# Kernel tuning notes

Hardware: AMD Instinct MI355X
Metric: run time of the kernel (lower is better)

The kernel has to match this reference:

```python
import jax, jax.numpy as jnp
import numpy as np

NEG = -1e6  # mask fill value used by d2l-style masked_softmax


def setup_inputs() -> dict:
    key = jax.random.key(0)
    kq, kk, kv, kl = jax.random.split(key, 4)
    B, Lq, Lk, D = 8, 2048, 2048, 64
    Q = jax.random.normal(kq, (B, Lq, D), dtype=jnp.float32)
    K = jax.random.normal(kk, (B, Lk, D), dtype=jnp.float32)
    V = jax.random.normal(kv, (B, Lk, D), dtype=jnp.float32)
    valid_len = jax.random.randint(kl, (B,), 1, Lk + 1, dtype=jnp.int64)
    return {"Q": Q, "K": K, "V": V, "valid_len": valid_len}


def reference(Q, K, V, valid_len):
    d = Q.shape[-1]
    scale = 1.0 / jnp.sqrt(jnp.asarray(d, dtype=Q.dtype))
    # scores: [B, Lq, Lk]
    S = jnp.einsum('bqd,bkd->bqk', Q, K) * scale
    Lk = K.shape[1]
    # per-batch key-length mask: position j valid iff j < valid_len[b]
    mask = jnp.arange(Lk)[None, None, :] < valid_len[:, None, None]
    S = jnp.where(mask, S, NEG)
    A = jax.nn.softmax(S, axis=-1)
    return jnp.einsum('bqk,bkd->bqd', A, V)
```

## Files before the change

### kernel.cpp

```cpp
#include <hip/hip_runtime.h>
#include <hip/hip_bf16.h>


constexpr int B_  = 8;
constexpr int L_  = 2048;
constexpr int D_  = 64;
constexpr int BQ  = 128;
constexpr int BK  = 64;
constexpr int LDK = 72;
constexpr int NQ  = L_ / BQ;

constexpr float QSCALE = 0.125f * 1.44269504088896340736f;

using bf16x8 = __attribute__((ext_vector_type(8))) __bf16;
using f32x4  = __attribute__((ext_vector_type(4))) float;

union frag_u { unsigned u[4]; bf16x8 v; };

#if __has_builtin(__builtin_amdgcn_exp2f)
#define EXP2(x) __builtin_amdgcn_exp2f(x)
#else
#define EXP2(x) exp2f(x)
#endif

__device__ __forceinline__ unsigned pack2(float lo, float hi) {
    __hip_bfloat162 h = __float22bfloat162_rn(make_float2(lo, hi));
    return *(unsigned*)&h;
}
__device__ __forceinline__ int sniff_valid(const int* vl, int b) {
    const int p1 = vl[1];
    return (p1 == 0) ? vl[2 * b] : vl[b];
}

__global__ __launch_bounds__(256, 2) void attn_fwd(
    const float* __restrict__ Q, const float* __restrict__ K,
    const float* __restrict__ V, const int* __restrict__ vl,
    float* __restrict__ O, float* __restrict__ Opart,
    float* __restrict__ lpart, int nsplit, int splitk)
{
    __shared__ __align__(16) unsigned short Ks[BK * LDK];
    __shared__ __align__(16) unsigned short Vt[D_ * LDK];
    __shared__ __align__(16) unsigned short Ps[4 * 32 * LDK];

    const int id   = blockIdx.x;
    const int qt   = id & (NQ - 1);
    const int b    = (id >> 4) & (B_ - 1);
    const int s    = id >> 7;
    const int tid  = threadIdx.x;
    const int wave = tid >> 6;
    const int lan  = tid & 15;
    const int quad = (tid >> 4) & 3;

    const int valid  = sniff_valid(vl, b);
    const int kstart = s * splitk;
    if (kstart >= valid) return;
    const int kend   = min(kstart + splitk, valid);
    const int ntiles = (kend - kstart + BK - 1) / BK;

    const float* Kg = K + (size_t)b * L_ * D_;
    const float* Vg = V + (size_t)b * L_ * D_;

    const int krow = tid >> 4, kc0 = (tid & 15) * 4;
    const int vk0  = (tid & 31) * 2, vd0 = (tid >> 5) * 8;

    float4 kr[4], vr[4];
    {
        const float* ks = Kg + (size_t)(kstart + krow) * D_ + kc0;
        #pragma unroll
        for (int p = 0; p < 4; ++p) kr[p] = *(const float4*)(ks + (size_t)p * 16 * D_);
        const float* vs = Vg + (size_t)(kstart + vk0) * D_ + vd0;
        vr[0] = *(const float4*)(vs);
        vr[1] = *(const float4*)(vs + 4);
        vr[2] = *(const float4*)(vs + D_);
        vr[3] = *(const float4*)(vs + D_ + 4);
    }

    bf16x8 aq[2][2];
    #pragma unroll
    for (int g = 0; g < 2; ++g) {
        const float* qs = Q + ((size_t)b * L_ + qt * BQ + wave * 32 + g * 16 + lan) * D_;
        float4 q0 = *(const float4*)(qs + quad * 8);
        float4 q1 = *(const float4*)(qs + quad * 8 + 4);
        float4 q2 = *(const float4*)(qs + 32 + quad * 8);
        float4 q3 = *(const float4*)(qs + 32 + quad * 8 + 4);
        frag_u f0, f1;
        f0.u[0] = pack2(q0.x * QSCALE, q0.y * QSCALE);
        f0.u[1] = pack2(q0.z * QSCALE, q0.w * QSCALE);
        f0.u[2] = pack2(q1.x * QSCALE, q1.y * QSCALE);
        f0.u[3] = pack2(q1.z * QSCALE, q1.w * QSCALE);
        f1.u[0] = pack2(q2.x * QSCALE, q2.y * QSCALE);
        f1.u[1] = pack2(q2.z * QSCALE, q2.w * QSCALE);
        f1.u[2] = pack2(q3.x * QSCALE, q3.y * QSCALE);
        f1.u[3] = pack2(q3.z * QSCALE, q3.w * QSCALE);
        aq[g][0] = f0.v;
        aq[g][1] = f1.v;
    }

    f32x4 oacc[2][4];
    #pragma unroll
    for (int g = 0; g < 2; ++g)
        #pragma unroll
        for (int c = 0; c < 4; ++c) oacc[g][c] = (f32x4){0.f, 0.f, 0.f, 0.f};
    float lsum[2] = {0.f, 0.f};

    unsigned short* Pw = &Ps[wave * 32 * LDK];

    for (int t = 0; t < ntiles; ++t) {
        const int kt = kstart + t * BK;
        __syncthreads();

        #pragma unroll
        for (int p = 0; p < 4; ++p) {
            uint2 w = make_uint2(pack2(kr[p].x, kr[p].y), pack2(kr[p].z, kr[p].w));
            *(uint2*)&Ks[(p * 16 + krow) * LDK + kc0] = w;
        }
        {
            const float* a = (const float*)&vr[0];
            const float* c = (const float*)&vr[2];
            #pragma unroll
            for (int j = 0; j < 8; ++j)
                *(unsigned*)&Vt[(vd0 + j) * LDK + vk0] = pack2(a[j], c[j]);
        }
        __syncthreads();

        if (t + 1 < ntiles) {
            const int kn = kt + BK;
            const float* ks = Kg + (size_t)(kn + krow) * D_ + kc0;
            #pragma unroll
            for (int p = 0; p < 4; ++p) kr[p] = *(const float4*)(ks + (size_t)p * 16 * D_);
            const float* vs = Vg + (size_t)(kn + vk0) * D_ + vd0;
            vr[0] = *(const float4*)(vs);
            vr[1] = *(const float4*)(vs + 4);
            vr[2] = *(const float4*)(vs + D_);
            vr[3] = *(const float4*)(vs + D_ + 4);
        }

        #pragma unroll
        for (int c = 0; c < 4; ++c) {
            bf16x8 ak0 = *(const bf16x8*)&Ks[(c*16 + lan) * LDK + quad * 8];
            bf16x8 ak1 = *(const bf16x8*)&Ks[(c*16 + lan) * LDK + 32 + quad * 8];
            f32x4 z0 = (f32x4){0.f, 0.f, 0.f, 0.f};
            f32x4 z1 = (f32x4){0.f, 0.f, 0.f, 0.f};
            z0 = __builtin_amdgcn_mfma_f32_16x16x32_bf16(ak0, aq[0][0], z0, 0, 0, 0);
            z1 = __builtin_amdgcn_mfma_f32_16x16x32_bf16(ak0, aq[1][0], z1, 0, 0, 0);
            z0 = __builtin_amdgcn_mfma_f32_16x16x32_bf16(ak1, aq[0][1], z0, 0, 0, 0);
            z1 = __builtin_amdgcn_mfma_f32_16x16x32_bf16(ak1, aq[1][1], z1, 0, 0, 0);

            const int kbase = kt + c * 16 + quad * 4;
            float p0[4], p1[4];
            #pragma unroll
            for (int r = 0; r < 4; ++r) {
                const bool ok = (kbase + r) < valid;
                p0[r] = ok ? EXP2(z0[r]) : 0.f;
                p1[r] = ok ? EXP2(z1[r]) : 0.f;
                lsum[0] += p0[r];
                lsum[1] += p1[r];
            }
            *(uint2*)&Pw[lan * LDK + c * 16 + quad * 4] =
                make_uint2(pack2(p0[0], p0[1]), pack2(p0[2], p0[3]));
            *(uint2*)&Pw[(16 + lan) * LDK + c * 16 + quad * 4] =
                make_uint2(pack2(p1[0], p1[1]), pack2(p1[2], p1[3]));
        }

        bf16x8 ap[2][2];
        #pragma unroll
        for (int g = 0; g < 2; ++g) {
            ap[g][0] = *(const bf16x8*)&Pw[(g*16 + lan) * LDK + quad * 8];
            ap[g][1] = *(const bf16x8*)&Pw[(g*16 + lan) * LDK + 32 + quad * 8];
        }
        #pragma unroll
        for (int c = 0; c < 4; ++c) {
            bf16x8 bv0 = *(const bf16x8*)&Vt[(c*16 + lan) * LDK + quad * 8];
            bf16x8 bv1 = *(const bf16x8*)&Vt[(c*16 + lan) * LDK + 32 + quad * 8];
            #pragma unroll
            for (int g = 0; g < 2; ++g) {
                oacc[g][c] = __builtin_amdgcn_mfma_f32_16x16x32_bf16(ap[g][0], bv0, oacc[g][c], 0, 0, 0);
                oacc[g][c] = __builtin_amdgcn_mfma_f32_16x16x32_bf16(ap[g][1], bv1, oacc[g][c], 0, 0, 0);
            }
        }
    }

    #pragma unroll
    for (int g = 0; g < 2; ++g) {
        lsum[g] += __shfl_xor(lsum[g], 16);
        lsum[g] += __shfl_xor(lsum[g], 32);
    }

    const int rowbase = qt * BQ + wave * 32;
    if (nsplit == 1) {
        #pragma unroll
        for (int g = 0; g < 2; ++g) {
            float inv[4];
            #pragma unroll
            for (int r = 0; r < 4; ++r)
                inv[r] = 1.0f / __shfl(lsum[g], quad * 4 + r);
            float* Og = O + ((size_t)b * L_ + rowbase + g * 16) * D_;
            #pragma unroll
            for (int c = 0; c < 4; ++c)
                #pragma unroll
                for (int r = 0; r < 4; ++r)
                    Og[(size_t)(quad * 4 + r) * D_ + c * 16 + lan] = oacc[g][c][r] * inv[r];
        }
    } else {
        #pragma unroll
        for (int g = 0; g < 2; ++g) {
            float* Og = Opart + ((size_t)s * B_ * L_ + (size_t)b * L_ + rowbase + g * 16) * D_;
            #pragma unroll
            for (int c = 0; c < 4; ++c)
                #pragma unroll
                for (int r = 0; r < 4; ++r)
                    Og[(size_t)(quad * 4 + r) * D_ + c * 16 + lan] = oacc[g][c][r];
            if (quad == 0)
                lpart[(size_t)s * B_ * L_ + (size_t)b * L_ + rowbase + g * 16 + lan] = lsum[g];
        }
    }
}

__global__ __launch_bounds__(256) void attn_combine(
    const float* __restrict__ Opart, const float* __restrict__ lpart,
    const int* __restrict__ vl, float* __restrict__ O,
    int nsplit, int splitk)
{
    const int idx = blockIdx.x * 256 + threadIdx.x;
    const int row = idx >> 4;
    const int b   = row >> 11;
    const int off = (idx & 15) * 4;
    const int valid = sniff_valid(vl, b);
    const int ns = min(nsplit, (valid + splitk - 1) / splitk);

    float Lsum = 0.f;
    float4 acc = make_float4(0.f, 0.f, 0.f, 0.f);
    for (int s = 0; s < ns; ++s) {
        Lsum += lpart[s * (B_ * L_) + row];
        float4 o4 = *(const float4*)&Opart[(size_t)s * (B_ * L_ * D_) + (size_t)row * D_ + off];
        acc.x += o4.x; acc.y += o4.y; acc.z += o4.z; acc.w += o4.w;
    }
    const float inv = 1.0f / Lsum;
    acc.x *= inv; acc.y *= inv; acc.z *= inv; acc.w *= inv;
    *(float4*)&O[(size_t)row * D_ + off] = acc;
}

extern "C" void kernel_launch(void* const* d_in, const int* in_sizes, int n_in,
                              void* d_out, int out_size, void* d_ws, size_t ws_size,
                              hipStream_t stream) {
    const float* Q  = (const float*)d_in[0];
    const float* K  = (const float*)d_in[1];
    const float* V  = (const float*)d_in[2];
    const int*   vl = (const int*)d_in[3];
    float* O = (float*)d_out;

    auto need = [](int n) {
        return (size_t)n * (B_ * L_ * D_ + B_ * L_) * sizeof(float);
    };
    int nsplit = 1;
    if      (ws_size >= need(4)) nsplit = 4;
    else if (ws_size >= need(2)) nsplit = 2;
    const int splitk = L_ / nsplit;

    float* Opart = (float*)d_ws;
    float* lpart = Opart + (size_t)nsplit * B_ * L_ * D_;

    attn_fwd<<<dim3(nsplit * B_ * NQ), 256, 0, stream>>>(
        Q, K, V, vl, O, Opart, lpart, nsplit, splitk);
    if (nsplit > 1)
        attn_combine<<<dim3((B_ * L_ * D_ / 4) / 256), 256, 0, stream>>>(
            Opart, lpart, vl, O, nsplit, splitk);
}
```

Baseline: 88.38 us.

## Use a persistent atomic work queue and allow an eight-way key split

The attention kernel becomes persistent. A fixed grid of 512 blocks pulls (split, batch, q-tile) work items from a global atomic ticket, which is zeroed with a memset before each launch. Items whose key range starts past the batch's valid length are skipped cheaply, so the blocks balance the uneven per-batch work dynamically. The key split can now go to 8 when the workspace allows. That gives finer-grained items, but more partial-output traffic and a longer combine pass, plus an extra memset and atomic per item.

```diff
diff --git a/kernel.cpp b/kernel.cpp
--- a/kernel.cpp
+++ b/kernel.cpp
@@ -9,6 +9,7 @@
 constexpr int BK  = 64;
 constexpr int LDK = 72;
 constexpr int NQ  = L_ / BQ;
+constexpr int NBLK = 512;
 
 constexpr float QSCALE = 0.125f * 1.44269504088896340736f;
 
@@ -36,183 +37,201 @@
     const float* __restrict__ Q, const float* __restrict__ K,
     const float* __restrict__ V, const int* __restrict__ vl,
     float* __restrict__ O, float* __restrict__ Opart,
-    float* __restrict__ lpart, int nsplit, int splitk)
+    float* __restrict__ lpart, int* __restrict__ ticket,
+    int nsplit, int splitk)
 {
     __shared__ __align__(16) unsigned short Ks[BK * LDK];
     __shared__ __align__(16) unsigned short Vt[D_ * LDK];
     __shared__ __align__(16) unsigned short Ps[4 * 32 * LDK];
-
-    const int id   = blockIdx.x;
-    const int qt   = id & (NQ - 1);
-    const int b    = (id >> 4) & (B_ - 1);
-    const int s    = id >> 7;
+    __shared__ int sh_item;
+
     const int tid  = threadIdx.x;
     const int wave = tid >> 6;
     const int lan  = tid & 15;
     const int quad = (tid >> 4) & 3;
 
-    const int valid  = sniff_valid(vl, b);
-    const int kstart = s * splitk;
-    if (kstart >= valid) return;
-    const int kend   = min(kstart + splitk, valid);
-    const int ntiles = (kend - kstart + BK - 1) / BK;
-
-    const float* Kg = K + (size_t)b * L_ * D_;
-    const float* Vg = V + (size_t)b * L_ * D_;
-
     const int krow = tid >> 4, kc0 = (tid & 15) * 4;
     const int vk0  = (tid & 31) * 2, vd0 = (tid >> 5) * 8;
 
-    float4 kr[4], vr[4];
-    {
-        const float* ks = Kg + (size_t)(kstart + krow) * D_ + kc0;
-        #pragma unroll
-        for (int p = 0; p < 4; ++p) kr[p] = *(const float4*)(ks + (size_t)p * 16 * D_);
-        const float* vs = Vg + (size_t)(kstart + vk0) * D_ + vd0;
-        vr[0] = *(const float4*)(vs);
-        vr[1] = *(const float4*)(vs + 4);
-        vr[2] = *(const float4*)(vs + D_);
-        vr[3] = *(const float4*)(vs + D_ + 4);
-    }
-
-    bf16x8 aq[2][2];
-    #pragma unroll
-    for (int g = 0; g < 2; ++g) {
-        const float* qs = Q + ((size_t)b * L_ + qt * BQ + wave * 32 + g * 16 + lan) * D_;
-        float4 q0 = *(const float4*)(qs + quad * 8);
-        float4 q1 = *(const float4*)(qs + quad * 8 + 4);
-        float4 q2 = *(const float4*)(qs + 32 + quad * 8);
-        float4 q3 = *(const float4*)(qs + 32 + quad * 8 + 4);
-        frag_u f0, f1;
-        f0.u[0] = pack2(q0.x * QSCALE, q0.y * QSCALE);
-        f0.u[1] = pack2(q0.z * QSCALE, q0.w * QSCALE);
-        f0.u[2] = pack2(q1.x * QSCALE, q1.y * QSCALE);
-        f0.u[3] = pack2(q1.z * QSCALE, q1.w * QSCALE);
-        f1.u[0] = pack2(q2.x * QSCALE, q2.y * QSCALE);
-        f1.u[1] = pack2(q2.z * QSCALE, q2.w * QSCALE);
-        f1.u[2] = pack2(q3.x * QSCALE, q3.y * QSCALE);
-        f1.u[3] = pack2(q3.z * QSCALE, q3.w * QSCALE);
-        aq[g][0] = f0.v;
-        aq[g][1] = f1.v;
-    }
-
-    f32x4 oacc[2][4];
-    #pragma unroll
-    for (int g = 0; g < 2; ++g)
-        #pragma unroll
-        for (int c = 0; c < 4; ++c) oacc[g][c] = (f32x4){0.f, 0.f, 0.f, 0.f};
-    float lsum[2] = {0.f, 0.f};
-
-    unsigned short* Pw = &Ps[wave * 32 * LDK];
-
-    for (int t = 0; t < ntiles; ++t) {
-        const int kt = kstart + t * BK;
+    const int nitems = nsplit * B_ * NQ;
+
+    for (;;) {
         __syncthreads();
-
-        #pragma unroll
-        for (int p = 0; p < 4; ++p) {
-            uint2 w = make_uint2(pack2(kr[p].x, kr[p].y), pack2(kr[p].z, kr[p].w));
-            *(uint2*)&Ks[(p * 16 + krow) * LDK + kc0] = w;
-        }
+        if (tid == 0) {
+            int it;
+            if (ticket) it = atomicAdd(ticket, 1);
+            else        it = blockIdx.x;
+            sh_item = it;
+        }
+        __syncthreads();
+        const int item = sh_item;
+        if (item >= nitems) break;
+
+        const int s  = item >> 7;
+        const int b  = (item >> 4) & (B_ - 1);
+        const int qt = item & (NQ - 1);
+
+        const int valid  = sniff_valid(vl, b);
+        const int kstart = s * splitk;
+        if (kstart >= valid) { if (!ticket) break; continue; }
+        const int kend   = min(kstart + splitk, valid);
+        const int ntiles = (kend - kstart + BK - 1) / BK;
+
+        const float* Kg = K + (size_t)b * L_ * D_;
+        const float* Vg = V + (size_t)b * L_ * D_;
+
+        float4 kr[4], vr[4];
         {
-            const float* a = (const float*)&vr[0];
-            const float* c = (const float*)&vr[2];
-            #pragma unroll
-            for (int j = 0; j < 8; ++j)
-                *(unsigned*)&Vt[(vd0 + j) * LDK + vk0] = pack2(a[j], c[j]);
-        }
-        __syncthreads();
-
-        if (t + 1 < ntiles) {
-            const int kn = kt + BK;
-            const float* ks = Kg + (size_t)(kn + krow) * D_ + kc0;
+            const float* ks = Kg + (size_t)(kstart + krow) * D_ + kc0;
             #pragma unroll
             for (int p = 0; p < 4; ++p) kr[p] = *(const float4*)(ks + (size_t)p * 16 * D_);
-            const float* vs = Vg + (size_t)(kn + vk0) * D_ + vd0;
+            const float* vs = Vg + (size_t)(kstart + vk0) * D_ + vd0;
             vr[0] = *(const float4*)(vs);
             vr[1] = *(const float4*)(vs + 4);
             vr[2] = *(const float4*)(vs + D_);
             vr[3] = *(const float4*)(vs + D_ + 4);
         }
 
-        #pragma unroll
-        for (int c = 0; c < 4; ++c) {
-            bf16x8 ak0 = *(const bf16x8*)&Ks[(c*16 + lan) * LDK + quad * 8];
-            bf16x8 ak1 = *(const bf16x8*)&Ks[(c*16 + lan) * LDK + 32 + quad * 8];
-            f32x4 z0 = (f32x4){0.f, 0.f, 0.f, 0.f};
-            f32x4 z1 = (f32x4){0.f, 0.f, 0.f, 0.f};
-            z0 = __builtin_amdgcn_mfma_f32_16x16x32_bf16(ak0, aq[0][0], z0, 0, 0, 0);
-            z1 = __builtin_amdgcn_mfma_f32_16x16x32_bf16(ak0, aq[1][0], z1, 0, 0, 0);
-            z0 = __builtin_amdgcn_mfma_f32_16x16x32_bf16(ak1, aq[0][1], z0, 0, 0, 0);
-            z1 = __builtin_amdgcn_mfma_f32_16x16x32_bf16(ak1, aq[1][1], z1, 0, 0, 0);
-
-            const int kbase = kt + c * 16 + quad * 4;
-            float p0[4], p1[4];
-            #pragma unroll
-            for (int r = 0; r < 4; ++r) {
-                const bool ok = (kbase + r) < valid;
-                p0[r] = ok ? EXP2(z0[r]) : 0.f;
-                p1[r] = ok ? EXP2(z1[r]) : 0.f;
-                lsum[0] += p0[r];
-                lsum[1] += p1[r];
-            }
-            *(uint2*)&Pw[lan * LDK + c * 16 + quad * 4] =
-                make_uint2(pack2(p0[0], p0[1]), pack2(p0[2], p0[3]));
-            *(uint2*)&Pw[(16 + lan) * LDK + c * 16 + quad * 4] =
-                make_uint2(pack2(p1[0], p1[1]), pack2(p1[2], p1[3]));
-        }
-
-        bf16x8 ap[2][2];
+        bf16x8 aq[2][2];
         #pragma unroll
         for (int g = 0; g < 2; ++g) {
-            ap[g][0] = *(const bf16x8*)&Pw[(g*16 + lan) * LDK + quad * 8];
-            ap[g][1] = *(const bf16x8*)&Pw[(g*16 + lan) * LDK + 32 + quad * 8];
-        }
+            const float* qs = Q + ((size_t)b * L_ + qt * BQ + wave * 32 + g * 16 + lan) * D_;
+            float4 q0 = *(const float4*)(qs + quad * 8);
+            float4 q1 = *(const float4*)(qs + quad * 8 + 4);
+            float4 q2 = *(const float4*)(qs + 32 + quad * 8);
+            float4 q3 = *(const float4*)(qs + 32 + quad * 8 + 4);
+            frag_u f0, f1;
+            f0.u[0] = pack2(q0.x * QSCALE, q0.y * QSCALE);
+            f0.u[1] = pack2(q0.z * QSCALE, q0.w * QSCALE);
+            f0.u[2] = pack2(q1.x * QSCALE, q1.y * QSCALE);
+            f0.u[3] = pack2(q1.z * QSCALE, q1.w * QSCALE);
+            f1.u[0] = pack2(q2.x * QSCALE, q2.y * QSCALE);
+            f1.u[1] = pack2(q2.z * QSCALE, q2.w * QSCALE);
+            f1.u[2] = pack2(q3.x * QSCALE, q3.y * QSCALE);
+            f1.u[3] = pack2(q3.z * QSCALE, q3.w * QSCALE);
+            aq[g][0] = f0.v;
+            aq[g][1] = f1.v;
+        }
+
+        f32x4 oacc[2][4];
         #pragma unroll
-        for (int c = 0; c < 4; ++c) {
-            bf16x8 bv0 = *(const bf16x8*)&Vt[(c*16 + lan) * LDK + quad * 8];
-            bf16x8 bv1 = *(const bf16x8*)&Vt[(c*16 + lan) * LDK + 32 + quad * 8];
+        for (int g = 0; g < 2; ++g)
+            #pragma unroll
+            for (int c = 0; c < 4; ++c) oacc[g][c] = (f32x4){0.f, 0.f, 0.f, 0.f};
+        float lsum[2] = {0.f, 0.f};
+
+        unsigned short* Pw = &Ps[wave * 32 * LDK];
+
+        for (int t = 0; t < ntiles; ++t) {
+            const int kt = kstart + t * BK;
+            __syncthreads();
+
+            #pragma unroll
+            for (int p = 0; p < 4; ++p) {
+                uint2 w = make_uint2(pack2(kr[p].x, kr[p].y), pack2(kr[p].z, kr[p].w));
+                *(uint2*)&Ks[(p * 16 + krow) * LDK + kc0] = w;
+            }
+            {
+                const float* a = (const float*)&vr[0];
+                const float* c = (const float*)&vr[2];
+                #pragma unroll
+                for (int j = 0; j < 8; ++j)
+                    *(unsigned*)&Vt[(vd0 + j) * LDK + vk0] = pack2(a[j], c[j]);
+            }
+            __syncthreads();
+
+            if (t + 1 < ntiles) {
+                const int kn = kt + BK;
+                const float* ks = Kg + (size_t)(kn + krow) * D_ + kc0;
+                #pragma unroll
+                for (int p = 0; p < 4; ++p) kr[p] = *(const float4*)(ks + (size_t)p * 16 * D_);
+                const float* vs = Vg + (size_t)(kn + vk0) * D_ + vd0;
+                vr[0] = *(const float4*)(vs);
+                vr[1] = *(const float4*)(vs + 4);
+                vr[2] = *(const float4*)(vs + D_);
+                vr[3] = *(const float4*)(vs + D_ + 4);
+            }
+
+            #pragma unroll
+            for (int c = 0; c < 4; ++c) {
+                bf16x8 ak0 = *(const bf16x8*)&Ks[(c*16 + lan) * LDK + quad * 8];
+                bf16x8 ak1 = *(const bf16x8*)&Ks[(c*16 + lan) * LDK + 32 + quad * 8];
+                f32x4 z0 = (f32x4){0.f, 0.f, 0.f, 0.f};
+                f32x4 z1 = (f32x4){0.f, 0.f, 0.f, 0.f};
+                z0 = __builtin_amdgcn_mfma_f32_16x16x32_bf16(ak0, aq[0][0], z0, 0, 0, 0);
+                z1 = __builtin_amdgcn_mfma_f32_16x16x32_bf16(ak0, aq[1][0], z1, 0, 0, 0);
+                z0 = __builtin_amdgcn_mfma_f32_16x16x32_bf16(ak1, aq[0][1], z0, 0, 0, 0);
+                z1 = __builtin_amdgcn_mfma_f32_16x16x32_bf16(ak1, aq[1][1], z1, 0, 0, 0);
+
+                const int kbase = kt + c * 16 + quad * 4;
+                float p0[4], p1[4];
+                #pragma unroll
+                for (int r = 0; r < 4; ++r) {
+                    const bool ok = (kbase + r) < valid;
+                    p0[r] = ok ? EXP2(z0[r]) : 0.f;
+                    p1[r] = ok ? EXP2(z1[r]) : 0.f;
+                    lsum[0] += p0[r];
+                    lsum[1] += p1[r];
+                }
+                *(uint2*)&Pw[lan * LDK + c * 16 + quad * 4] =
+                    make_uint2(pack2(p0[0], p0[1]), pack2(p0[2], p0[3]));
+                *(uint2*)&Pw[(16 + lan) * LDK + c * 16 + quad * 4] =
+                    make_uint2(pack2(p1[0], p1[1]), pack2(p1[2], p1[3]));
+            }
+
+            bf16x8 ap[2][2];
             #pragma unroll
             for (int g = 0; g < 2; ++g) {
-                oacc[g][c] = __builtin_amdgcn_mfma_f32_16x16x32_bf16(ap[g][0], bv0, oacc[g][c], 0, 0, 0);
-                oacc[g][c] = __builtin_amdgcn_mfma_f32_16x16x32_bf16(ap[g][1], bv1, oacc[g][c], 0, 0, 0);
-            }
-        }
-    }
-
-    #pragma unroll
-    for (int g = 0; g < 2; ++g) {
-        lsum[g] += __shfl_xor(lsum[g], 16);
-        lsum[g] += __shfl_xor(lsum[g], 32);
-    }
-
-    const int rowbase = qt * BQ + wave * 32;
-    if (nsplit == 1) {
+                ap[g][0] = *(const bf16x8*)&Pw[(g*16 + lan) * LDK + quad * 8];
+                ap[g][1] = *(const bf16x8*)&Pw[(g*16 + lan) * LDK + 32 + quad * 8];
+            }
+            #pragma unroll
+            for (int c = 0; c < 4; ++c) {
+                bf16x8 bv0 = *(const bf16x8*)&Vt[(c*16 + lan) * LDK + quad * 8];
+                bf16x8 bv1 = *(const bf16x8*)&Vt[(c*16 + lan) * LDK + 32 + quad * 8];
+                #pragma unroll
+                for (int g = 0; g < 2; ++g) {
+                    oacc[g][c] = __builtin_amdgcn_mfma_f32_16x16x32_bf16(ap[g][0], bv0, oacc[g][c], 0, 0, 0);
+                    oacc[g][c] = __builtin_amdgcn_mfma_f32_16x16x32_bf16(ap[g][1], bv1, oacc[g][c], 0, 0, 0);
+                }
+            }
+        }
+
         #pragma unroll
         for (int g = 0; g < 2; ++g) {
-            float inv[4];
-            #pragma unroll
-            for (int r = 0; r < 4; ++r)
-                inv[r] = 1.0f / __shfl(lsum[g], quad * 4 + r);
-            float* Og = O + ((size_t)b * L_ + rowbase + g * 16) * D_;
-            #pragma unroll
-            for (int c = 0; c < 4; ++c)
+            lsum[g] += __shfl_xor(lsum[g], 16);
+            lsum[g] += __shfl_xor(lsum[g], 32);
+        }
+
+        const int rowbase = qt * BQ + wave * 32;
+        if (nsplit == 1) {
+            #pragma unroll
+            for (int g = 0; g < 2; ++g) {
+                float inv[4];
                 #pragma unroll
                 for (int r = 0; r < 4; ++r)
-                    Og[(size_t)(quad * 4 + r) * D_ + c * 16 + lan] = oacc[g][c][r] * inv[r];
-        }
-    } else {
-        #pragma unroll
-        for (int g = 0; g < 2; ++g) {
-            float* Og = Opart + ((size_t)s * B_ * L_ + (size_t)b * L_ + rowbase + g * 16) * D_;
-            #pragma unroll
-            for (int c = 0; c < 4; ++c)
-                #pragma unroll
-                for (int r = 0; r < 4; ++r)
-                    Og[(size_t)(quad * 4 + r) * D_ + c * 16 + lan] = oacc[g][c][r];
-            if (quad == 0)
-                lpart[(size_t)s * B_ * L_ + (size_t)b * L_ + rowbase + g * 16 + lan] = lsum[g];
-        }
+                    inv[r] = 1.0f / __shfl(lsum[g], quad * 4 + r);
+                float* Og = O + ((size_t)b * L_ + rowbase + g * 16) * D_;
+                #pragma unroll
+                for (int c = 0; c < 4; ++c)
+                    #pragma unroll
+                    for (int r = 0; r < 4; ++r)
+                        Og[(size_t)(quad * 4 + r) * D_ + c * 16 + lan] = oacc[g][c][r] * inv[r];
+            }
+        } else {
+            #pragma unroll
+            for (int g = 0; g < 2; ++g) {
+                float* Og = Opart + ((size_t)s * B_ * L_ + (size_t)b * L_ + rowbase + g * 16) * D_;
+                #pragma unroll
+                for (int c = 0; c < 4; ++c)
+                    #pragma unroll
+                    for (int r = 0; r < 4; ++r)
+                        Og[(size_t)(quad * 4 + r) * D_ + c * 16 + lan] = oacc[g][c][r];
+                if (quad == 0)
+                    lpart[(size_t)s * B_ * L_ + (size_t)b * L_ + rowbase + g * 16 + lan] = lsum[g];
+            }
+        }
+        if (!ticket) break;
     }
 }
 
@@ -250,19 +269,26 @@
     float* O = (float*)d_out;
 
     auto need = [](int n) {
-        return (size_t)n * (B_ * L_ * D_ + B_ * L_) * sizeof(float);
+        return (size_t)n * (B_ * L_ * D_ + B_ * L_) * sizeof(float) + 64;
     };
     int nsplit = 1;
-    if      (ws_size >= need(4)) nsplit = 4;
+    if      (ws_size >= need(8)) nsplit = 8;
+    else if (ws_size >= need(4)) nsplit = 4;
     else if (ws_size >= need(2)) nsplit = 2;
     const int splitk = L_ / nsplit;
 
     float* Opart = (float*)d_ws;
     float* lpart = Opart + (size_t)nsplit * B_ * L_ * D_;
-
-    attn_fwd<<<dim3(nsplit * B_ * NQ), 256, 0, stream>>>(
-        Q, K, V, vl, O, Opart, lpart, nsplit, splitk);
-    if (nsplit > 1)
+    int*   ticket = (int*)(lpart + (size_t)nsplit * B_ * L_);
+
+    if (nsplit > 1) {
+        hipMemsetAsync(ticket, 0, sizeof(int), stream);
+        attn_fwd<<<dim3(NBLK), 256, 0, stream>>>(
+            Q, K, V, vl, O, Opart, lpart, ticket, nsplit, splitk);
         attn_combine<<<dim3((B_ * L_ * D_ / 4) / 256), 256, 0, stream>>>(
             Opart, lpart, vl, O, nsplit, splitk);
-}
+    } else {
+        attn_fwd<<<dim3(B_ * NQ), 256, 0, stream>>>(
+            Q, K, V, vl, O, Opart, lpart, nullptr, 1, splitk);
+    }
+}
```

Result: slower. 99.18 us (+12.2%).
